# Optimization experiments

Hardware: AMD Instinct MI355X
Metric: run time of the kernel (lower is better)

## Reference

```python
import jax, jax.numpy as jnp
import numpy as np

DIM = 2048
ORDER = 1
# upper-triangular index pairs (i<j), row-major over i then j — matches torch loop order
_IU_ROWS, _IU_COLS = np.triu_indices(DIM, k=1)


def setup_inputs() -> dict:
    key = jax.random.key(0)
    k1, k2 = jax.random.split(key)
    num_params = DIM * (DIM - 1) // 2
    x = jax.random.normal(k1, (4, 4096, DIM), dtype=jnp.float32)
    angles = jax.random.normal(k2, (num_params,), dtype=jnp.float32) * 0.01
    bias = jnp.zeros((DIM,), dtype=jnp.float32)
    return {"x": x, "angles": angles, "bias": bias}


def _skew_symmetric(angles):
    # A[i,j] = angles[k], A[j,i] = -angles[k] for upper-tri (i<j)
    A = jnp.zeros((DIM, DIM), dtype=angles.dtype)
    A = A.at[_IU_ROWS, _IU_COLS].set(angles)
    return A - A.T


def _cayley_approx(A, order=ORDER):
    # W = (I + A + ... + A^order) @ (I + A)
    I = jnp.eye(DIM, dtype=A.dtype)
    inv_approx = I
    A_power = A
    for _ in range(order):
        inv_approx = inv_approx + A_power
        A_power = A_power @ A
    return inv_approx @ (I + A)


def reference(x, angles, bias):
    A = _skew_symmetric(angles)
    W = _cayley_approx(A)
    # [b, s, d] @ [d, d] -> [b, s, d]
    out = jnp.einsum('bsd,de->bse', x, W) + bias
    return out
```

## Files before the change

### kernel.cpp

```cpp
#include <hip/hip_runtime.h>
#include <stdint.h>

#define DIM 2048

typedef short short8 __attribute__((ext_vector_type(8)));
typedef float f32x4 __attribute__((ext_vector_type(4)));

__device__ __forceinline__ unsigned short f2bf(float f) {
    union { float f; unsigned int u; } v;
    v.f = f;
    unsigned int r = v.u + 0x7FFFu + ((v.u >> 16) & 1u);
    return (unsigned short)(r >> 16);
}
__device__ __forceinline__ float bf2f(unsigned short u) {
    union { unsigned int u; float f; } v;
    v.u = ((unsigned int)u) << 16;
    return v.f;
}

__device__ __forceinline__ void async16(const unsigned short* g, unsigned short* l) {
    __builtin_amdgcn_global_load_lds(
        (__attribute__((address_space(1))) void*)(uintptr_t)g,
        (__attribute__((address_space(3))) void*)(uintptr_t)l,
        16, 0, 0);
}

#define NCVT 32768

__global__ __launch_bounds__(256) void prep_fused(const float* __restrict__ x,
                                                  unsigned short* __restrict__ xbf,
                                                  const float* __restrict__ ang,
                                                  unsigned short* __restrict__ A) {
    __shared__ float tile[64][65];
    if (blockIdx.x < NCVT) {
        const int i = (blockIdx.x * 256 + threadIdx.x) * 4;
        const float4 v = *(const float4*)(x + i);
        ushort4 o;
        o.x = f2bf(v.x); o.y = f2bf(v.y); o.z = f2bf(v.z); o.w = f2bf(v.w);
        *(ushort4*)(xbf + i) = o;
        return;
    }
    int b = blockIdx.x - NCVT;
    int ti = 0, rem = b;
    while (rem >= 32 - ti) { rem -= 32 - ti; ++ti; }
    const int tj = ti + rem;
    const int t  = threadIdx.x;
    const int lj = t & 63;
    const int lw = t >> 6;
    const bool diag = (ti == tj);

#pragma unroll
    for (int m = 0; m < 16; ++m) {
        const int li = lw * 16 + m;
        const int i = ti * 64 + li;
        const int j = tj * 64 + lj;
        float v = 0.0f;
        if (i < j) v = ang[i * (4095 - i) / 2 + (j - i - 1)];
        tile[li][lj] = v;
    }
    __syncthreads();

#pragma unroll
    for (int m = 0; m < 16; ++m) {
        const int li = lw * 16 + m;
        float v;
        if (diag) {
            if (li < lj)      v =  tile[li][lj];
            else if (li > lj) v = -tile[lj][li];
            else              v = 0.0f;
        } else {
            v = tile[li][lj];
        }
        A[(size_t)(ti * 64 + li) * DIM + tj * 64 + lj] = f2bf(v);
    }
    if (!diag) {
#pragma unroll
        for (int m = 0; m < 16; ++m) {
            const int li = lw * 16 + m;
            A[(size_t)(tj * 64 + li) * DIM + ti * 64 + lj] = f2bf(-tile[lj][li]);
        }
    }
}

__global__ __launch_bounds__(256) void gemm_s64(
        const unsigned short* __restrict__ A,
        unsigned short* __restrict__ Wt) {
    __shared__ __align__(16) unsigned short ldsA[128 * 64];
    __shared__ __align__(16) unsigned short ldsB[64 * 64];
    const int K = DIM, N = DIM;

    const int t    = threadIdx.x;
    const int flat = blockIdx.y * 32 + blockIdx.x;
    const int swz  = (flat & 7) * 64 + (flat >> 3);
    const int bn   = (swz & 31) * 64;
    const int bm   = (swz >> 5) * 128;
    const int lane = t & 63;
    const int wave = t >> 6;
    const int waveM = (wave >> 1) * 64;
    const int waveN = (wave & 1) * 32;
    const int fm = lane & 15;
    const int fq = lane >> 4;

    f32x4 acc[4][2];
#pragma unroll
    for (int i = 0; i < 4; ++i)
#pragma unroll
        for (int j = 0; j < 2; ++j)
            acc[i][j] = (f32x4){0.f, 0.f, 0.f, 0.f};

    const int trow   = t >> 3;
    const int tchunk = (t & 7) ^ (trow & 7);
    const unsigned short* gA = A + (size_t)(bm + trow) * K + tchunk * 8;
    const unsigned short* gB = A + (size_t)(bn + trow) * K + tchunk * 8;
    const size_t rowskip = (size_t)32 * K;
    unsigned short* lA = ldsA + t * 8;
    unsigned short* lB = ldsB + t * 8;

    for (int kt = 0; kt < K; kt += 64) {
        __syncthreads();
        async16(gA + kt,                lA);
        async16(gA + kt +     rowskip,  lA + 2048);
        async16(gA + kt + 2 * rowskip,  lA + 4096);
        async16(gA + kt + 3 * rowskip,  lA + 6144);
        async16(gB + kt,                lB);
        async16(gB + kt +     rowskip,  lB + 2048);
        __syncthreads();

#pragma unroll
        for (int ks = 0; ks < 2; ++ks) {
            short8 af[4], bfv[2];
#pragma unroll
            for (int i = 0; i < 4; ++i) {
                const int rowA = waveM + i * 16 + fm;
                af[i] = *(const short8*)(ldsA + rowA * 64 + (((ks << 2) + fq) ^ (rowA & 7)) * 8);
            }
#pragma unroll
            for (int j = 0; j < 2; ++j) {
                const int rowB = waveN + j * 16 + fm;
                bfv[j] = *(const short8*)(ldsB + rowB * 64 + (((ks << 2) + fq) ^ (rowB & 7)) * 8);
            }
#pragma unroll
            for (int i = 0; i < 4; ++i)
#pragma unroll
                for (int j = 0; j < 2; ++j)
                    acc[i][j] = __builtin_amdgcn_mfma_f32_16x16x32_bf16(
                        af[i], bfv[j], acc[i][j], 0, 0, 0);
        }
    }

#pragma unroll
    for (int i = 0; i < 4; ++i) {
#pragma unroll
        for (int j = 0; j < 2; ++j) {
            const int col = bn + waveN + j * 16 + fm;
#pragma unroll
            for (int r = 0; r < 4; ++r) {
                const int row = bm + waveM + i * 16 + fq * 4 + r;
                const float a = bf2f(A[(size_t)row * N + col]);
                const float w = (row == col ? 1.0f : 0.0f) - 2.0f * a - acc[i][j][r];
                Wt[(size_t)row * N + col] = f2bf(w);
            }
        }
    }
}


#define WAITV(N) asm volatile("s_waitcnt vmcnt(" #N ")" ::: "memory")
#define BAR() do { asm volatile("" ::: "memory"); __builtin_amdgcn_s_barrier(); asm volatile("" ::: "memory"); } while (0)

#define STG_A(BUF, R0, KT) async16(gA + (size_t)(R0) * 2048 + (KT), &ldsA[BUF][(R0) * 64 + t * 8])
#define STG_B(BUF, R0, KT) async16(gB + (size_t)(R0) * 2048 + (KT), &ldsB[BUF][(R0) * 64 + t * 8])

#define READ_A_(BUF, IH) do { \
    _Pragma("unroll") \
    for (int ii = 0; ii < 4; ++ii) { \
        const int row  = waveM + (IH) * 64 + ii * 16 + fm; \
        const int base = row * 64; \
        af[ii][0] = *(const short8*)(&ldsA[BUF][base + ((fq    ) ^ (row & 7)) * 8]); \
        af[ii][1] = *(const short8*)(&ldsA[BUF][base + ((fq + 4) ^ (row & 7)) * 8]); \
    } } while (0)

#define READ_B_(BUF, JH) do { \
    _Pragma("unroll") \
    for (int jj = 0; jj < 2; ++jj) { \
        const int row  = (JH) * 128 + wn * 32 + jj * 16 + fm; \
        const int base = row * 64; \
        bfr[JH][jj][0] = *(const short8*)(&ldsB[BUF][base + ((fq    ) ^ (row & 7)) * 8]); \
        bfr[JH][jj][1] = *(const short8*)(&ldsB[BUF][base + ((fq + 4) ^ (row & 7)) * 8]); \
    } } while (0)

#define MMAQ(IH, JH) do { \
    __builtin_amdgcn_s_setprio(1); \
    _Pragma("unroll") \
    for (int ks = 0; ks < 2; ++ks) \
    _Pragma("unroll") \
    for (int ii = 0; ii < 4; ++ii) \
    _Pragma("unroll") \
    for (int jj = 0; jj < 2; ++jj) \
        acc[(IH) * 4 + ii][(JH) * 2 + jj] = __builtin_amdgcn_mfma_f32_16x16x32_bf16( \
            af[ii][ks], bfr[JH][jj][ks], acc[(IH) * 4 + ii][(JH) * 2 + jj], 0, 0, 0); \
    __builtin_amdgcn_s_setprio(0); \
} while (0)

#define TILE(BUF, KTN, PRE, VN, NXT) do { \
     \
    BAR(); \
    if (PRE) { STG_A(BUF, 0, KTN); STG_A(BUF, 128, KTN); STG_B(BUF, 0, KTN); STG_B(BUF, 64, KTN); } \
    MMAQ(0, 0); \
    READ_B_(BUF, 1); \
     \
    BAR(); \
    if (PRE) { STG_B(BUF, 128, KTN); STG_B(BUF, 192, KTN); } \
    MMAQ(0, 1); \
    READ_A_(BUF, 1); \
     \
    WAITV(VN); \
    BAR(); \
    if (PRE) { STG_A(BUF, 64, KTN); STG_A(BUF, 192, KTN); } \
    MMAQ(1, 0); \
    if (NXT) READ_B_((BUF) ^ 1, 0); \
     \
    BAR(); \
    MMAQ(1, 1); \
    if (NXT) READ_A_((BUF) ^ 1, 0); \
} while (0)

#define TILE_LAST(BUF) do { \
    BAR(); MMAQ(0, 0); READ_B_(BUF, 1); \
    BAR(); MMAQ(0, 1); READ_A_(BUF, 1); \
    BAR(); MMAQ(1, 0); \
    MMAQ(1, 1); \
} while (0)

__global__ __launch_bounds__(512, 2) void gemm_main(
        const unsigned short* __restrict__ Aop,
        const unsigned short* __restrict__ Bop,
        int M, int N, int K,
        const float* __restrict__ bias,
        float* __restrict__ out) {
    __shared__ __align__(16) unsigned short ldsA[2][256 * 64];
    __shared__ __align__(16) unsigned short ldsB[2][256 * 64];

    const int t    = threadIdx.x;
    const int flat = blockIdx.y * 8 + blockIdx.x;
    const int swz  = (flat & 7) * 64 + (flat >> 3);
    const int bn   = (swz & 7) * 256;
    const int bm   = (swz >> 3) * 256;
    const int lane = t & 63;
    const int wave = t >> 6;
    const int wm   = wave >> 2;
    const int wn   = wave & 3;
    const int waveM = wm * 128;
    const int fm = lane & 15;
    const int fq = lane >> 4;

    f32x4 acc[8][4];
#pragma unroll
    for (int i = 0; i < 8; ++i)
#pragma unroll
        for (int j = 0; j < 4; ++j)
            acc[i][j] = (f32x4){0.f, 0.f, 0.f, 0.f};

    short8 af[4][2];
    short8 bfr[2][2][2];

    const int trow   = t >> 3;
    const int tchunk = (t & 7) ^ (trow & 7);
    const unsigned short* gA = Aop + (size_t)(bm + trow) * 2048 + tchunk * 8;
    const unsigned short* gB = Bop + (size_t)(bn + trow) * 2048 + tchunk * 8;

    STG_A(0, 0, 0);   STG_A(0, 128, 0);  STG_B(0, 0, 0);   STG_B(0, 64, 0);
    STG_B(0, 128, 0); STG_B(0, 192, 0);  STG_A(0, 64, 0);  STG_A(0, 192, 0);
    STG_A(1, 0, 64);  STG_A(1, 128, 64); STG_B(1, 0, 64);  STG_B(1, 64, 64);
    STG_B(1, 128, 64);STG_B(1, 192, 64); STG_A(1, 64, 64); STG_A(1, 192, 64);
    WAITV(8);
    BAR();
    READ_A_(0, 0);
    READ_B_(0, 0);

#pragma unroll 1
    for (int it = 0; it < 15; ++it) {
        const int kt = it * 128;
        TILE(0, kt + 128, 1, 6, 1);
        TILE(1, kt + 192, 1, 6, 1);
    }
    TILE(0, 0, 0, 0, 1);
    TILE_LAST(1);

#pragma unroll
    for (int i = 0; i < 8; ++i) {
        const int row0 = bm + waveM + i * 16 + fq * 4;
#pragma unroll
        for (int j = 0; j < 4; ++j) {
            const int col = bn + (j >> 1) * 128 + wn * 32 + (j & 1) * 16 + fm;
            const float b = bias[col];
#pragma unroll
            for (int r = 0; r < 4; ++r)
                out[(size_t)(row0 + r) * 2048 + col] = acc[i][j][r] + b;
        }
    }
}

extern "C" void kernel_launch(void* const* d_in, const int* in_sizes, int n_in,
                              void* d_out, int out_size, void* d_ws, size_t ws_size,
                              hipStream_t stream) {
    const float* x      = (const float*)d_in[0];
    const float* angles = (const float*)d_in[1];
    const float* bias   = (const float*)d_in[2];
    float* out = (float*)d_out;

    char* ws = (char*)d_ws;
    unsigned short* Abf = (unsigned short*)ws;
    unsigned short* Wt  = (unsigned short*)(ws + (8u << 20));
    unsigned short* xbf = (unsigned short*)(ws + (16u << 20));

    const int M = 4 * 4096;

    prep_fused<<<NCVT + 528, 256, 0, stream>>>(x, xbf, angles, Abf);

    gemm_s64<<<dim3(DIM / 64, DIM / 128), 256, 0, stream>>>(Abf, Wt);

    gemm_main<<<dim3(DIM / 256, M / 256), 512, 0, stream>>>(
        xbf, Wt, M, DIM, DIM, bias, out);
}
```

Measured before the change: 368.9 us.

## Switch main GEMM to 32x32x16 MFMA and fuse x conversion into A^2 kernel

```diff
diff --git a/kernel.cpp b/kernel.cpp
--- a/kernel.cpp
+++ b/kernel.cpp
@@ -5,6 +5,7 @@
 
 typedef short short8 __attribute__((ext_vector_type(8)));
 typedef float f32x4 __attribute__((ext_vector_type(4)));
+typedef float f32x16 __attribute__((ext_vector_type(16)));
 
 __device__ __forceinline__ unsigned short f2bf(float f) {
     union { float f; unsigned int u; } v;
@@ -25,22 +26,10 @@
         16, 0, 0);
 }
 
-#define NCVT 32768
-
-__global__ __launch_bounds__(256) void prep_fused(const float* __restrict__ x,
-                                                  unsigned short* __restrict__ xbf,
-                                                  const float* __restrict__ ang,
-                                                  unsigned short* __restrict__ A) {
+__global__ __launch_bounds__(256) void build_A_tiled(const float* __restrict__ ang,
+                                                     unsigned short* __restrict__ A) {
     __shared__ float tile[64][65];
-    if (blockIdx.x < NCVT) {
-        const int i = (blockIdx.x * 256 + threadIdx.x) * 4;
-        const float4 v = *(const float4*)(x + i);
-        ushort4 o;
-        o.x = f2bf(v.x); o.y = f2bf(v.y); o.z = f2bf(v.z); o.w = f2bf(v.w);
-        *(ushort4*)(xbf + i) = o;
-        return;
-    }
-    int b = blockIdx.x - NCVT;
+    int b = blockIdx.x;
     int ti = 0, rem = b;
     while (rem >= 32 - ti) { rem -= 32 - ti; ++ti; }
     const int tj = ti + rem;
@@ -82,15 +71,26 @@
     }
 }
 
-__global__ __launch_bounds__(256) void gemm_s64(
+__global__ __launch_bounds__(256) void s64_cvt(
         const unsigned short* __restrict__ A,
-        unsigned short* __restrict__ Wt) {
+        unsigned short* __restrict__ Wt,
+        const float* __restrict__ x,
+        unsigned short* __restrict__ xbf) {
     __shared__ __align__(16) unsigned short ldsA[128 * 64];
     __shared__ __align__(16) unsigned short ldsB[64 * 64];
+
+    if (blockIdx.x >= 512) {
+        const int i = ((blockIdx.x - 512) * 256 + threadIdx.x) * 4;
+        const float4 v = *(const float4*)(x + i);
+        ushort4 o;
+        o.x = f2bf(v.x); o.y = f2bf(v.y); o.z = f2bf(v.z); o.w = f2bf(v.w);
+        *(ushort4*)(xbf + i) = o;
+        return;
+    }
+
     const int K = DIM, N = DIM;
-
     const int t    = threadIdx.x;
-    const int flat = blockIdx.y * 32 + blockIdx.x;
+    const int flat = blockIdx.x;
     const int swz  = (flat & 7) * 64 + (flat >> 3);
     const int bn   = (swz & 31) * 64;
     const int bm   = (swz >> 5) * 128;
@@ -173,32 +173,31 @@
 
 #define READ_A_(BUF, IH) do { \
     _Pragma("unroll") \
-    for (int ii = 0; ii < 4; ++ii) { \
-        const int row  = waveM + (IH) * 64 + ii * 16 + fm; \
+    for (int ii = 0; ii < 2; ++ii) { \
+        const int row  = waveM + ((IH) * 2 + ii) * 32 + r32; \
         const int base = row * 64; \
-        af[ii][0] = *(const short8*)(&ldsA[BUF][base + ((fq    ) ^ (row & 7)) * 8]); \
-        af[ii][1] = *(const short8*)(&ldsA[BUF][base + ((fq + 4) ^ (row & 7)) * 8]); \
+        _Pragma("unroll") \
+        for (int ks = 0; ks < 4; ++ks) \
+            af[ii][ks] = *(const short8*)(&ldsA[BUF][base + (((ks << 1) + hi) ^ (row & 7)) * 8]); \
     } } while (0)
 
 #define READ_B_(BUF, JH) do { \
-    _Pragma("unroll") \
-    for (int jj = 0; jj < 2; ++jj) { \
-        const int row  = (JH) * 128 + wn * 32 + jj * 16 + fm; \
+    { \
+        const int row  = (JH) * 128 + wn * 32 + r32; \
         const int base = row * 64; \
-        bfr[JH][jj][0] = *(const short8*)(&ldsB[BUF][base + ((fq    ) ^ (row & 7)) * 8]); \
-        bfr[JH][jj][1] = *(const short8*)(&ldsB[BUF][base + ((fq + 4) ^ (row & 7)) * 8]); \
+        _Pragma("unroll") \
+        for (int ks = 0; ks < 4; ++ks) \
+            bfr[JH][ks] = *(const short8*)(&ldsB[BUF][base + (((ks << 1) + hi) ^ (row & 7)) * 8]); \
     } } while (0)
 
 #define MMAQ(IH, JH) do { \
     __builtin_amdgcn_s_setprio(1); \
     _Pragma("unroll") \
-    for (int ks = 0; ks < 2; ++ks) \
+    for (int ks = 0; ks < 4; ++ks) \
     _Pragma("unroll") \
-    for (int ii = 0; ii < 4; ++ii) \
-    _Pragma("unroll") \
-    for (int jj = 0; jj < 2; ++jj) \
-        acc[(IH) * 4 + ii][(JH) * 2 + jj] = __builtin_amdgcn_mfma_f32_16x16x32_bf16( \
-            af[ii][ks], bfr[JH][jj][ks], acc[(IH) * 4 + ii][(JH) * 2 + jj], 0, 0, 0); \
+    for (int ii = 0; ii < 2; ++ii) \
+        acc[(IH) * 2 + ii][JH] = __builtin_amdgcn_mfma_f32_32x32x16_bf16( \
+            af[ii][ks], bfr[JH][ks], acc[(IH) * 2 + ii][JH], 0, 0, 0); \
     __builtin_amdgcn_s_setprio(0); \
 } while (0)
 
@@ -251,18 +250,20 @@
     const int wm   = wave >> 2;
     const int wn   = wave & 3;
     const int waveM = wm * 128;
-    const int fm = lane & 15;
-    const int fq = lane >> 4;
-
-    f32x4 acc[8][4];
-#pragma unroll
-    for (int i = 0; i < 8; ++i)
-#pragma unroll
-        for (int j = 0; j < 4; ++j)
-            acc[i][j] = (f32x4){0.f, 0.f, 0.f, 0.f};
-
-    short8 af[4][2];
-    short8 bfr[2][2][2];
+    const int r32  = lane & 31;
+    const int hi   = lane >> 5;
+
+    f32x16 acc[4][2];
+#pragma unroll
+    for (int i = 0; i < 4; ++i)
+#pragma unroll
+        for (int j = 0; j < 2; ++j)
+#pragma unroll
+            for (int r = 0; r < 16; ++r)
+                acc[i][j][r] = 0.f;
+
+    short8 af[2][4];
+    short8 bfr[2][4];
 
     const int trow   = t >> 3;
     const int tchunk = (t & 7) ^ (trow & 7);
@@ -288,15 +289,17 @@
     TILE_LAST(1);
 
 #pragma unroll
-    for (int i = 0; i < 8; ++i) {
-        const int row0 = bm + waveM + i * 16 + fq * 4;
-#pragma unroll
-        for (int j = 0; j < 4; ++j) {
-            const int col = bn + (j >> 1) * 128 + wn * 32 + (j & 1) * 16 + fm;
+    for (int i = 0; i < 4; ++i) {
+        const int rowb = bm + waveM + i * 32 + 4 * hi;
+#pragma unroll
+        for (int j = 0; j < 2; ++j) {
+            const int col = bn + j * 128 + wn * 32 + r32;
             const float b = bias[col];
 #pragma unroll
-            for (int r = 0; r < 4; ++r)
-                out[(size_t)(row0 + r) * 2048 + col] = acc[i][j][r] + b;
+            for (int r = 0; r < 16; ++r) {
+                const int row = rowb + (r & 3) + 8 * (r >> 2);
+                out[(size_t)row * 2048 + col] = acc[i][j][r] + b;
+            }
         }
     }
 }
@@ -316,9 +319,9 @@
 
     const int M = 4 * 4096;
 
-    prep_fused<<<NCVT + 528, 256, 0, stream>>>(x, xbf, angles, Abf);
-
-    gemm_s64<<<dim3(DIM / 64, DIM / 128), 256, 0, stream>>>(Abf, Wt);
+    build_A_tiled<<<528, 256, 0, stream>>>(angles, Abf);
+
+    s64_cvt<<<512 + 32768, 256, 0, stream>>>(Abf, Wt, x, xbf);
 
     gemm_main<<<dim3(DIM / 256, M / 256), 512, 0, stream>>>(
         xbf, Wt, M, DIM, DIM, bias, out);
```

After: 379.9 us. 3.0% more time.
